# Optimization experiments

Measured on AMD Instinct MI355X. Metric: run time of the kernel, lower is better.

The kernel has to match this reference:

```python
import jax, jax.numpy as jnp
import numpy as np
from jax import lax

REPR, ACT, HID = 256, 2, 512
BN_EPS = 1e-5


def setup_inputs() -> dict:
    key = jax.random.key(0)
    ks = jax.random.split(key, 12)
    B, H, W, Tm1 = 512, 64, 64, 16
    d_in = REPR + ACT
    s = lambda k, shape, scale: jax.random.normal(k, shape, dtype=jnp.float32) * scale
    return {
        "init_state": jax.random.normal(ks[0], (B, 2, H, W), dtype=jnp.float32),
        "actions": jax.random.normal(ks[1], (B, Tm1, ACT), dtype=jnp.float32),
        "conv_w": s(ks[2], (16, 2, 3, 3), (1.0 / np.sqrt(2 * 9))),
        "bn_gamma": jnp.ones((16,), jnp.float32),
        "bn_beta": jnp.zeros((16,), jnp.float32),
        "enc_fc_w": s(ks[3], (REPR, 16), (1.0 / np.sqrt(16))),
        "enc_fc_b": s(ks[4], (REPR,), 0.01),
        "gru_w_ih": s(ks[5], (3 * HID, d_in), (1.0 / np.sqrt(HID))),
        "gru_w_hh": s(ks[6], (3 * HID, HID), (1.0 / np.sqrt(HID))),
        "gru_b_ih": s(ks[7], (3 * HID,), (1.0 / np.sqrt(HID))),
        "gru_b_hh": s(ks[8], (3 * HID,), (1.0 / np.sqrt(HID))),
        "pred_fc_w": s(ks[9], (REPR, HID), (1.0 / np.sqrt(HID))),
        "pred_fc_b": s(ks[10], (REPR,), 0.01),
    }


def _encoder(x, conv_w, bn_gamma, bn_beta, enc_fc_w, enc_fc_b):
    # Conv2d(2->16, 3x3, stride 1, pad 1, no bias), NCHW
    y = lax.conv_general_dilated(x, conv_w, (1, 1), "SAME",
                                 dimension_numbers=("NCHW", "OIHW", "NCHW"))
    # BatchNorm2d in training mode: batch statistics over (N, H, W)
    mean = jnp.mean(y, axis=(0, 2, 3), keepdims=True)
    var = jnp.var(y, axis=(0, 2, 3), keepdims=True)
    y = (y - mean) * lax.rsqrt(var + BN_EPS)
    y = y * bn_gamma[None, :, None, None] + bn_beta[None, :, None, None]
    y = jax.nn.relu(y)
    # MaxPool2d(2, 2)
    y = lax.reduce_window(y, -jnp.inf, lax.max, (1, 1, 2, 2), (1, 1, 2, 2), "VALID")
    # AdaptiveAvgPool2d((1,1)) + flatten
    y = jnp.mean(y, axis=(2, 3))  # (B, 16)
    return y @ enc_fc_w.T + enc_fc_b  # (B, repr_dim)


def reference(init_state, actions, conv_w, bn_gamma, bn_beta, enc_fc_w, enc_fc_b,
              gru_w_ih, gru_w_hh, gru_b_ih, gru_b_hh, pred_fc_w, pred_fc_b):
    B = init_state.shape[0]
    s0 = _encoder(init_state, conv_w, bn_gamma, bn_beta, enc_fc_w, enc_fc_b)  # (B, R)

    def step(carry, u_t):
        s_prev, h = carry
        x = jnp.concatenate([s_prev, u_t], axis=-1)          # (B, R+A)
        gx = x @ gru_w_ih.T + gru_b_ih                        # (B, 3H)
        gh = h @ gru_w_hh.T + gru_b_hh                        # (B, 3H)
        gx_r, gx_z, gx_n = jnp.split(gx, 3, axis=-1)
        gh_r, gh_z, gh_n = jnp.split(gh, 3, axis=-1)
        r = jax.nn.sigmoid(gx_r + gh_r)
        z = jax.nn.sigmoid(gx_z + gh_z)
        n = jnp.tanh(gx_n + r * gh_n)
        h_new = (1.0 - z) * n + z * h
        s_pred = jax.nn.relu(h_new @ pred_fc_w.T + pred_fc_b)  # (B, R)
        return (s_pred, h_new), s_pred

    h0 = jnp.zeros((B, HID), dtype=s0.dtype)
    u_seq = jnp.transpose(actions, (1, 0, 2))  # (T-1, B, A)
    _, preds = lax.scan(step, (s0, h0), u_seq)  # preds: (T-1, B, R)
    pred_encs = jnp.concatenate([s0[None], preds], axis=0)  # (T, B, R)
    return jnp.transpose(pred_encs, (1, 0, 2))  # (B, T, R)
```

## Files before the change

### kernel.cpp

```cpp
#include <hip/hip_runtime.h>
#include <hip/hip_bf16.h>
#include <math.h>

#define TM1 16
#define TT 17

typedef __attribute__((ext_vector_type(8))) __bf16 bf16x8;
typedef __attribute__((ext_vector_type(4))) float f32x4;

#define OFF_BSTATS 0
#define OFF_SPB    16384
#define OFF_PWB    81920
#define OFF_WIHB   147456
#define OFF_WHHB   344064
#define OFF_HB     737280

#define IMG_STRIDE 67
#define IMG_CI (66 * IMG_STRIDE)

__global__ __launch_bounds__(256) void enc_stats_prep(
    const float* __restrict__ x, const float* __restrict__ cw,
    float* __restrict__ bstats,
    const float* __restrict__ wih, const float* __restrict__ whh,
    const float* __restrict__ pw,
    __hip_bfloat16* __restrict__ wihb, __hip_bfloat16* __restrict__ whhb,
    __hip_bfloat16* __restrict__ pwb) {
  {
    const int n1 = 1536 * 256, n2 = 1536 * 512, n3 = 256 * 512;
    int i = blockIdx.x * 256 + threadIdx.x;
    int st = gridDim.x * 256;
    for (int j = i; j < n1 + n2 + n3; j += st) {
      if (j < n1) {
        int r = j >> 8, c = j & 255;
        wihb[j] = __float2bfloat16(wih[r * 258 + c]);
      } else if (j < n1 + n2) {
        int k = j - n1;
        whhb[k] = __float2bfloat16(whh[k]);
      } else {
        int k = j - n1 - n2;
        pwb[k] = __float2bfloat16(pw[k]);
      }
    }
  }

  __shared__ float imgp[2 * IMG_CI];
  __shared__ float reds[4][16], redq[4][16];
  const int b = blockIdx.x, tid = threadIdx.x;
  const int wv = tid >> 6;
  for (int i = tid; i < 2 * IMG_CI; i += 256) imgp[i] = 0.0f;
  __syncthreads();
  const float* xb = x + b * 8192;
  for (int i = tid; i < 8192; i += 256) {
    int ci = i >> 12, rem = i & 4095, y = rem >> 6, xx = rem & 63;
    imgp[ci * IMG_CI + (y + 1) * IMG_STRIDE + (xx + 1)] = xb[i];
  }
  __syncthreads();

  const int py = tid >> 3;
  const int cb = (tid & 7) << 3;

  float s[16], q[16];
#pragma unroll
  for (int c = 0; c < 16; ++c) { s[c] = 0.0f; q[c] = 0.0f; }

#pragma unroll 1
  for (int op = 0; op < 2; ++op) {
    const int ic = cb + 4 * op;
    float rv[2][4][6];
#pragma unroll
    for (int ci = 0; ci < 2; ++ci)
#pragma unroll
      for (int dy = 0; dy < 4; ++dy)
#pragma unroll
        for (int j = 0; j < 6; ++j)
          rv[ci][dy][j] = imgp[ci * IMG_CI + (2 * py + dy) * IMG_STRIDE + ic + j];
#pragma unroll
    for (int c4 = 0; c4 < 4; ++c4) {
      float a[4][8];
#pragma unroll
      for (int ch = 0; ch < 4; ++ch)
#pragma unroll
        for (int j = 0; j < 8; ++j) a[ch][j] = 0.0f;
#pragma unroll
      for (int ci = 0; ci < 2; ++ci) {
        float wk[4][9];
#pragma unroll
        for (int ch = 0; ch < 4; ++ch)
#pragma unroll
          for (int k = 0; k < 9; ++k)
            wk[ch][k] = cw[(c4 * 4 + ch) * 18 + ci * 9 + k];
#pragma unroll
        for (int ry = 0; ry < 2; ++ry)
#pragma unroll
          for (int rx = 0; rx < 4; ++rx)
#pragma unroll
            for (int ch = 0; ch < 4; ++ch) {
              float acc = a[ch][ry * 4 + rx];
#pragma unroll
              for (int dy = 0; dy < 3; ++dy) {
                acc = fmaf(wk[ch][dy * 3 + 0], rv[ci][ry + dy][rx + 0], acc);
                acc = fmaf(wk[ch][dy * 3 + 1], rv[ci][ry + dy][rx + 1], acc);
                acc = fmaf(wk[ch][dy * 3 + 2], rv[ci][ry + dy][rx + 2], acc);
              }
              a[ch][ry * 4 + rx] = acc;
            }
      }
#pragma unroll
      for (int ch = 0; ch < 4; ++ch)
#pragma unroll
        for (int j = 0; j < 8; ++j) {
          const float v = a[ch][j];
          s[c4 * 4 + ch] += v;
          q[c4 * 4 + ch] = fmaf(v, v, q[c4 * 4 + ch]);
        }
    }
  }

#pragma unroll
  for (int c = 0; c < 16; ++c) {
    float sv = s[c], qv = q[c];
#pragma unroll
    for (int off = 32; off >= 1; off >>= 1) {
      sv += __shfl_down(sv, off);
      qv += __shfl_down(qv, off);
    }
    if ((tid & 63) == 0) { reds[wv][c] = sv; redq[wv][c] = qv; }
  }
  __syncthreads();
  if (tid < 16)
    bstats[b * 32 + tid] = reds[0][tid] + reds[1][tid] + reds[2][tid] + reds[3][tid];
  else if (tid < 32) {
    int c = tid - 16;
    bstats[b * 32 + tid] = redq[0][c] + redq[1][c] + redq[2][c] + redq[3][c];
  }
}

__global__ __launch_bounds__(256) void enc_finish(const float* __restrict__ x,
                                                  const float* __restrict__ cw,
                                                  const float* __restrict__ bstats,
                                                  const float* __restrict__ gamma,
                                                  const float* __restrict__ beta,
                                                  const float* __restrict__ fcw,
                                                  const float* __restrict__ fcb,
                                                  __hip_bfloat16* __restrict__ spb,
                                                  float* __restrict__ out) {
  __shared__ float imgp[2 * IMG_CI];
  __shared__ float red[4][16];
  __shared__ float plds[16];
  __shared__ float statsL[32];
  __shared__ float racc[8][32];
  const int b = blockIdx.x, tid = threadIdx.x;
  const int wv = tid >> 6;

  {
    const int c = tid & 31, part = tid >> 5;
    float s = 0;
    for (int bb = part; bb < 512; bb += 8) s += bstats[bb * 32 + c];
    racc[part][c] = s;
  }
  for (int i = tid; i < 2 * IMG_CI; i += 256) imgp[i] = 0.0f;
  __syncthreads();
  if (tid < 32) {
    float v = 0;
#pragma unroll
    for (int p = 0; p < 8; ++p) v += racc[p][tid];
    statsL[tid] = v;
  }
  const float* xb = x + b * 8192;
  for (int i = tid; i < 8192; i += 256) {
    int ci = i >> 12, rem = i & 4095, y = rem >> 6, xx = rem & 63;
    imgp[ci * IMG_CI + (y + 1) * IMG_STRIDE + (xx + 1)] = xb[i];
  }
  __syncthreads();

  const float invN = 1.0f / (512.0f * 4096.0f);
  const int py = tid >> 3;
  const int cb = (tid & 7) << 3;

  float psum[16];
#pragma unroll
  for (int c = 0; c < 16; ++c) psum[c] = 0.0f;

#pragma unroll 1
  for (int op = 0; op < 2; ++op) {
    const int ic = cb + 4 * op;
    float rv[2][4][6];
#pragma unroll
    for (int ci = 0; ci < 2; ++ci)
#pragma unroll
      for (int dy = 0; dy < 4; ++dy)
#pragma unroll
        for (int j = 0; j < 6; ++j)
          rv[ci][dy][j] = imgp[ci * IMG_CI + (2 * py + dy) * IMG_STRIDE + ic + j];
#pragma unroll
    for (int c4 = 0; c4 < 4; ++c4) {
      float a[4][8];
#pragma unroll
      for (int ch = 0; ch < 4; ++ch)
#pragma unroll
        for (int j = 0; j < 8; ++j) a[ch][j] = 0.0f;
#pragma unroll
      for (int ci = 0; ci < 2; ++ci) {
        float wk[4][9];
#pragma unroll
        for (int ch = 0; ch < 4; ++ch)
#pragma unroll
          for (int k = 0; k < 9; ++k)
            wk[ch][k] = cw[(c4 * 4 + ch) * 18 + ci * 9 + k];
#pragma unroll
        for (int ry = 0; ry < 2; ++ry)
#pragma unroll
          for (int rx = 0; rx < 4; ++rx)
#pragma unroll
            for (int ch = 0; ch < 4; ++ch) {
              float acc = a[ch][ry * 4 + rx];
#pragma unroll
              for (int dy = 0; dy < 3; ++dy) {
                acc = fmaf(wk[ch][dy * 3 + 0], rv[ci][ry + dy][rx + 0], acc);
                acc = fmaf(wk[ch][dy * 3 + 1], rv[ci][ry + dy][rx + 1], acc);
                acc = fmaf(wk[ch][dy * 3 + 2], rv[ci][ry + dy][rx + 2], acc);
              }
              a[ch][ry * 4 + rx] = acc;
            }
      }
#pragma unroll
      for (int ch = 0; ch < 4; ++ch) {
        const int c = c4 * 4 + ch;
        const float m = statsL[c] * invN;
        const float var = statsL[16 + c] * invN - m * m;
        const float isd = rsqrtf(var + 1e-5f);
        const float sc = gamma[c] * isd;
        const float sh = beta[c] - m * sc;
#pragma unroll
        for (int j = 0; j < 2; ++j) {
          const float v00 = fmaxf(fmaf(a[ch][2 * j + 0], sc, sh), 0.0f);
          const float v01 = fmaxf(fmaf(a[ch][2 * j + 1], sc, sh), 0.0f);
          const float v10 = fmaxf(fmaf(a[ch][4 + 2 * j + 0], sc, sh), 0.0f);
          const float v11 = fmaxf(fmaf(a[ch][4 + 2 * j + 1], sc, sh), 0.0f);
          psum[c] += fmaxf(fmaxf(v00, v01), fmaxf(v10, v11));
        }
      }
    }
  }

#pragma unroll
  for (int c = 0; c < 16; ++c) {
    float v = psum[c];
#pragma unroll
    for (int off = 32; off >= 1; off >>= 1) v += __shfl_down(v, off);
    if ((tid & 63) == 0) red[wv][c] = v;
  }
  __syncthreads();
  if (tid < 16)
    plds[tid] = (red[0][tid] + red[1][tid] + red[2][tid] + red[3][tid]) * (1.0f / 1024.0f);
  __syncthreads();

  float acc = fcb[tid];
#pragma unroll
  for (int c = 0; c < 16; ++c) acc = fmaf(plds[c], fcw[tid * 16 + c], acc);
  spb[b * 256 + tid] = __float2bfloat16(acc);
  out[(b * TT + 0) * 256 + tid] = acc;
}

__global__ __launch_bounds__(384) void gru_v2(
    const __hip_bfloat16* __restrict__ spb,
    const __hip_bfloat16* __restrict__ hb_in,
    __hip_bfloat16* __restrict__ hb_out,
    const __hip_bfloat16* __restrict__ wihb,
    const __hip_bfloat16* __restrict__ whhb,
    const float* __restrict__ wih,
    const float* __restrict__ actions,
    const float* __restrict__ bih, const float* __restrict__ bhh,
    int t) {
  __shared__ __hip_bfloat16 sF[8 * 64 * 8];
  __shared__ __hip_bfloat16 hF[16 * 64 * 8];
  __shared__ float accL[4][2][256];
  const int tid = threadIdx.x;
  const int w = tid / 64, lane = tid & 63;
  const int l15 = lane & 15, hi = lane >> 4;
  const int cg = blockIdx.x, band = blockIdx.y;
  const int row0 = band * 16;
  const int ct = w & 1, g = w >> 1;

  for (int i = tid; i < 512; i += 384) {
    int kk = i >> 6, ln = i & 63;
    *(bf16x8*)(sF + i * 8) =
        *(const bf16x8*)(spb + (row0 + (ln & 15)) * 256 + kk * 32 + (ln >> 4) * 8);
  }
  if (t > 0) {
    for (int i = tid; i < 1024; i += 384) {
      int kk = i >> 6, ln = i & 63;
      *(bf16x8*)(hF + i * 8) =
          *(const bf16x8*)(hb_in + (row0 + (ln & 15)) * 512 + kk * 32 + (ln >> 4) * 8);
    }
  }
  __syncthreads();

  const int cj = cg * 32 + ct * 16;
  f32x4 accS = {0.f, 0.f, 0.f, 0.f}, accH = accS;
  {
    const __hip_bfloat16* B = wihb + (g * 512 + cj + l15) * 256 + hi * 8;
#pragma unroll
    for (int kk = 0; kk < 8; ++kk) {
      bf16x8 a = *(const bf16x8*)(sF + (kk * 64 + lane) * 8);
      accS = __builtin_amdgcn_mfma_f32_16x16x32_bf16(a, *(const bf16x8*)(B + kk * 32),
                                                     accS, 0, 0, 0);
    }
  }
  if (t > 0) {
    const __hip_bfloat16* B = whhb + (g * 512 + cj + l15) * 512 + hi * 8;
#pragma unroll
    for (int kk = 0; kk < 16; ++kk) {
      bf16x8 a = *(const bf16x8*)(hF + (kk * 64 + lane) * 8);
      accH = __builtin_amdgcn_mfma_f32_16x16x32_bf16(a, *(const bf16x8*)(B + kk * 32),
                                                     accH, 0, 0, 0);
    }
  }
  if (g < 2) {
#pragma unroll
    for (int i = 0; i < 4; ++i)
      accL[g][ct][(hi * 4 + i) * 16 + l15] = accS[i] + accH[i];
  } else {
#pragma unroll
    for (int i = 0; i < 4; ++i) {
      accL[2][ct][(hi * 4 + i) * 16 + l15] = accS[i];
      accL[3][ct][(hi * 4 + i) * 16 + l15] = accH[i];
    }
  }
  __syncthreads();

  if (w < 2) {
    f32x4 vR = *(const f32x4*)&accL[0][w][lane * 4];
    f32x4 vZ = *(const f32x4*)&accL[1][w][lane * 4];
    f32x4 vXN = *(const f32x4*)&accL[2][w][lane * 4];
    f32x4 vHN = *(const f32x4*)&accL[3][w][lane * 4];
    const int r = lane >> 2;
    const int row = row0 + r;
    const float u0 = actions[row * 32 + t * 2 + 0];
    const float u1 = actions[row * 32 + t * 2 + 1];
#pragma unroll
    for (int j = 0; j < 4; ++j) {
      const int c = (lane & 3) * 4 + j;
      const int col = cg * 32 + w * 16 + c;
      const float br = bih[col] + bhh[col];
      const float bz = bih[512 + col] + bhh[512 + col];
      const float bxn = bih[1024 + col];
      const float bhn = bhh[1024 + col];
      const float wur = wih[col * 258 + 256], wvr = wih[col * 258 + 257];
      const float wuz = wih[(512 + col) * 258 + 256], wvz = wih[(512 + col) * 258 + 257];
      const float wun = wih[(1024 + col) * 258 + 256], wvn = wih[(1024 + col) * 258 + 257];
      const float gr = vR[j] + br + u0 * wur + u1 * wvr;
      const float gz = vZ[j] + bz + u0 * wuz + u1 * wvz;
      const float gxn = vXN[j] + bxn + u0 * wun + u1 * wvn;
      const float ghn = vHN[j] + bhn;
      const float rg = 1.0f / (1.0f + __expf(-gr));
      const float zg = 1.0f / (1.0f + __expf(-gz));
      float xn = gxn + rg * ghn;
      xn = fminf(fmaxf(xn, -15.0f), 15.0f);
      const float e = __expf(2.0f * xn);
      const float ng = (e - 1.0f) / (e + 1.0f);
      const float hp = (t > 0) ? (float)hb_in[row * 512 + col] : 0.0f;
      const float hnv = (1.0f - zg) * ng + zg * hp;
      hb_out[row * 512 + col] = __float2bfloat16(hnv);
    }
  }
}

__global__ __launch_bounds__(256) void pred_v2(
    const __hip_bfloat16* __restrict__ hb,
    const __hip_bfloat16* __restrict__ pwb,
    const float* __restrict__ pb,
    float* __restrict__ out,
    __hip_bfloat16* __restrict__ spb,
    int slot) {
  __shared__ float accL[4][256];
  const int tid = threadIdx.x;
  const int w = tid >> 6, lane = tid & 63;
  const int l15 = lane & 15, hi = lane >> 4;
  const int pcg = blockIdx.x, band = blockIdx.y;
  const int row0 = band * 16, pc0 = pcg * 16;
  f32x4 acc = {0.f, 0.f, 0.f, 0.f};
  const __hip_bfloat16* A = hb + (row0 + l15) * 512 + w * 128 + hi * 8;
  const __hip_bfloat16* B = pwb + (pc0 + l15) * 512 + w * 128 + hi * 8;
#pragma unroll
  for (int kk = 0; kk < 4; ++kk)
    acc = __builtin_amdgcn_mfma_f32_16x16x32_bf16(*(const bf16x8*)(A + kk * 32),
                                                  *(const bf16x8*)(B + kk * 32),
                                                  acc, 0, 0, 0);
#pragma unroll
  for (int i = 0; i < 4; ++i) accL[w][(hi * 4 + i) * 16 + l15] = acc[i];
  __syncthreads();
  if (w == 0) {
    f32x4 p0 = *(const f32x4*)&accL[0][lane * 4];
    f32x4 p1 = *(const f32x4*)&accL[1][lane * 4];
    f32x4 p2 = *(const f32x4*)&accL[2][lane * 4];
    f32x4 p3 = *(const f32x4*)&accL[3][lane * 4];
    const int r = lane >> 2;
    const int row = row0 + r;
    float4 ov;
    float* po = &ov.x;
#pragma unroll
    for (int j = 0; j < 4; ++j) {
      const int c = (lane & 3) * 4 + j;
      const int col = pc0 + c;
      float v = p0[j] + p1[j] + p2[j] + p3[j] + pb[col];
      v = fmaxf(v, 0.0f);
      po[j] = v;
      spb[row * 256 + col] = __float2bfloat16(v);
    }
    *(float4*)(out + ((size_t)row * TT + slot) * 256 + pc0 + (lane & 3) * 4) = ov;
  }
}

extern "C" void kernel_launch(void* const* d_in, const int* in_sizes, int n_in,
                              void* d_out, int out_size, void* d_ws, size_t ws_size,
                              hipStream_t stream) {
  const float* x       = (const float*)d_in[0];
  const float* actions = (const float*)d_in[1];
  const float* cw      = (const float*)d_in[2];
  const float* gamma   = (const float*)d_in[3];
  const float* beta    = (const float*)d_in[4];
  const float* fcw     = (const float*)d_in[5];
  const float* fcb     = (const float*)d_in[6];
  const float* wih     = (const float*)d_in[7];
  const float* whh     = (const float*)d_in[8];
  const float* bih     = (const float*)d_in[9];
  const float* bhh     = (const float*)d_in[10];
  const float* pw      = (const float*)d_in[11];
  const float* pb      = (const float*)d_in[12];
  float* out = (float*)d_out;
  float* ws  = (float*)d_ws;

  float* bstats = ws + OFF_BSTATS;
  __hip_bfloat16* spb  = (__hip_bfloat16*)(ws + OFF_SPB);
  __hip_bfloat16* pwb  = (__hip_bfloat16*)(ws + OFF_PWB);
  __hip_bfloat16* wihb = (__hip_bfloat16*)(ws + OFF_WIHB);
  __hip_bfloat16* whhb = (__hip_bfloat16*)(ws + OFF_WHHB);
  __hip_bfloat16* hb0  = (__hip_bfloat16*)(ws + OFF_HB);
  __hip_bfloat16* hb1  = hb0 + 512 * 512;

  enc_stats_prep<<<dim3(512), dim3(256), 0, stream>>>(x, cw, bstats, wih, whh, pw,
                                                      wihb, whhb, pwb);
  enc_finish<<<dim3(512), dim3(256), 0, stream>>>(x, cw, bstats, gamma, beta, fcw, fcb,
                                                  spb, out);
  for (int t = 0; t < TM1; ++t) {
    __hip_bfloat16* hbi = (t & 1) ? hb1 : hb0;
    __hip_bfloat16* hbo = (t & 1) ? hb0 : hb1;
    gru_v2<<<dim3(16, 32), dim3(384), 0, stream>>>(spb, hbi, hbo, wihb, whhb,
                                                   wih, actions, bih, bhh, t);
    pred_v2<<<dim3(16, 32), dim3(256), 0, stream>>>(hbo, pwb, pb, out, spb, t + 1);
  }
}
```

Measured before the change: 364.1 us.

## Split encoder into row slabs, separate stats reduction, fuse encoder FC into first GRU step

```diff
diff --git a/kernel.cpp b/kernel.cpp
--- a/kernel.cpp
+++ b/kernel.cpp
@@ -9,14 +9,30 @@
 typedef __attribute__((ext_vector_type(4))) float f32x4;
 
 #define OFF_BSTATS 0
-#define OFF_SPB    16384
-#define OFF_PWB    81920
-#define OFF_WIHB   147456
-#define OFF_WHHB   344064
-#define OFF_HB     737280
+#define OFF_STATS  65536
+#define OFF_POOLED 65568
+#define OFF_SPB    98336
+#define OFF_PWB    163872
+#define OFF_WIHB   229408
+#define OFF_WHHB   426016
+#define OFF_HB     819232
 
 #define IMG_STRIDE 67
-#define IMG_CI (66 * IMG_STRIDE)
+#define SLAB_ROWS 18
+#define IMG_CI (SLAB_ROWS * IMG_STRIDE)
+
+__device__ __forceinline__ void stage_slab(float* __restrict__ imgp,
+                                           const float* __restrict__ xb, int slab, int tid) {
+  for (int i = tid; i < 2 * SLAB_ROWS * 66; i += 256) {
+    const int ci = i / (SLAB_ROWS * 66);
+    const int rem = i - ci * (SLAB_ROWS * 66);
+    const int lr = rem / 66, c = rem - lr * 66;
+    const int gr = slab * 16 - 1 + lr;
+    float v = 0.0f;
+    if (gr >= 0 && gr < 64 && c >= 1 && c <= 64) v = xb[ci * 4096 + gr * 64 + (c - 1)];
+    imgp[ci * IMG_CI + lr * IMG_STRIDE + c] = v;
+  }
+}
 
 __global__ __launch_bounds__(256) void enc_stats_prep(
     const float* __restrict__ x, const float* __restrict__ cw,
@@ -45,75 +61,67 @@
 
   __shared__ float imgp[2 * IMG_CI];
   __shared__ float reds[4][16], redq[4][16];
-  const int b = blockIdx.x, tid = threadIdx.x;
+  const int tid = threadIdx.x;
+  const int b = blockIdx.x >> 2, slab = blockIdx.x & 3;
   const int wv = tid >> 6;
-  for (int i = tid; i < 2 * IMG_CI; i += 256) imgp[i] = 0.0f;
-  __syncthreads();
-  const float* xb = x + b * 8192;
-  for (int i = tid; i < 8192; i += 256) {
-    int ci = i >> 12, rem = i & 4095, y = rem >> 6, xx = rem & 63;
-    imgp[ci * IMG_CI + (y + 1) * IMG_STRIDE + (xx + 1)] = xb[i];
-  }
-  __syncthreads();
-
-  const int py = tid >> 3;
-  const int cb = (tid & 7) << 3;
+  stage_slab(imgp, x + b * 8192, slab, tid);
+  __syncthreads();
+
+  const int pr = tid >> 5;
+  const int pc = tid & 31;
+
+  float rv[2][4][4];
+#pragma unroll
+  for (int ci = 0; ci < 2; ++ci)
+#pragma unroll
+    for (int dy = 0; dy < 4; ++dy)
+#pragma unroll
+      for (int j = 0; j < 4; ++j)
+        rv[ci][dy][j] = imgp[ci * IMG_CI + (2 * pr + dy) * IMG_STRIDE + 2 * pc + j];
 
   float s[16], q[16];
 #pragma unroll
   for (int c = 0; c < 16; ++c) { s[c] = 0.0f; q[c] = 0.0f; }
 
-#pragma unroll 1
-  for (int op = 0; op < 2; ++op) {
-    const int ic = cb + 4 * op;
-    float rv[2][4][6];
-#pragma unroll
-    for (int ci = 0; ci < 2; ++ci)
-#pragma unroll
-      for (int dy = 0; dy < 4; ++dy)
-#pragma unroll
-        for (int j = 0; j < 6; ++j)
-          rv[ci][dy][j] = imgp[ci * IMG_CI + (2 * py + dy) * IMG_STRIDE + ic + j];
-#pragma unroll
-    for (int c4 = 0; c4 < 4; ++c4) {
-      float a[4][8];
+#pragma unroll
+  for (int c4 = 0; c4 < 4; ++c4) {
+    float a[4][4];
+#pragma unroll
+    for (int ch = 0; ch < 4; ++ch)
+#pragma unroll
+      for (int p = 0; p < 4; ++p) a[ch][p] = 0.0f;
+#pragma unroll
+    for (int ci = 0; ci < 2; ++ci) {
+      float wk[4][9];
 #pragma unroll
       for (int ch = 0; ch < 4; ++ch)
 #pragma unroll
-        for (int j = 0; j < 8; ++j) a[ch][j] = 0.0f;
-#pragma unroll
-      for (int ci = 0; ci < 2; ++ci) {
-        float wk[4][9];
-#pragma unroll
-        for (int ch = 0; ch < 4; ++ch)
-#pragma unroll
-          for (int k = 0; k < 9; ++k)
-            wk[ch][k] = cw[(c4 * 4 + ch) * 18 + ci * 9 + k];
-#pragma unroll
-        for (int ry = 0; ry < 2; ++ry)
-#pragma unroll
-          for (int rx = 0; rx < 4; ++rx)
-#pragma unroll
-            for (int ch = 0; ch < 4; ++ch) {
-              float acc = a[ch][ry * 4 + rx];
-#pragma unroll
-              for (int dy = 0; dy < 3; ++dy) {
-                acc = fmaf(wk[ch][dy * 3 + 0], rv[ci][ry + dy][rx + 0], acc);
-                acc = fmaf(wk[ch][dy * 3 + 1], rv[ci][ry + dy][rx + 1], acc);
-                acc = fmaf(wk[ch][dy * 3 + 2], rv[ci][ry + dy][rx + 2], acc);
-              }
-              a[ch][ry * 4 + rx] = acc;
+        for (int k = 0; k < 9; ++k)
+          wk[ch][k] = cw[(c4 * 4 + ch) * 18 + ci * 9 + k];
+#pragma unroll
+      for (int ry = 0; ry < 2; ++ry)
+#pragma unroll
+        for (int rx = 0; rx < 2; ++rx)
+#pragma unroll
+          for (int ch = 0; ch < 4; ++ch) {
+            float acc = a[ch][ry * 2 + rx];
+#pragma unroll
+            for (int dy = 0; dy < 3; ++dy) {
+              acc = fmaf(wk[ch][dy * 3 + 0], rv[ci][ry + dy][rx + 0], acc);
+              acc = fmaf(wk[ch][dy * 3 + 1], rv[ci][ry + dy][rx + 1], acc);
+              acc = fmaf(wk[ch][dy * 3 + 2], rv[ci][ry + dy][rx + 2], acc);
             }
+            a[ch][ry * 2 + rx] = acc;
+          }
+    }
+#pragma unroll
+    for (int ch = 0; ch < 4; ++ch)
+#pragma unroll
+      for (int p = 0; p < 4; ++p) {
+        const float v = a[ch][p];
+        s[c4 * 4 + ch] += v;
+        q[c4 * 4 + ch] = fmaf(v, v, q[c4 * 4 + ch]);
       }
-#pragma unroll
-      for (int ch = 0; ch < 4; ++ch)
-#pragma unroll
-        for (int j = 0; j < 8; ++j) {
-          const float v = a[ch][j];
-          s[c4 * 4 + ch] += v;
-          q[c4 * 4 + ch] = fmaf(v, v, q[c4 * 4 + ch]);
-        }
-    }
   }
 
 #pragma unroll
@@ -128,118 +136,106 @@
   }
   __syncthreads();
   if (tid < 16)
-    bstats[b * 32 + tid] = reds[0][tid] + reds[1][tid] + reds[2][tid] + reds[3][tid];
+    bstats[blockIdx.x * 32 + tid] = reds[0][tid] + reds[1][tid] + reds[2][tid] + reds[3][tid];
   else if (tid < 32) {
     int c = tid - 16;
-    bstats[b * 32 + tid] = redq[0][c] + redq[1][c] + redq[2][c] + redq[3][c];
-  }
-}
-
-__global__ __launch_bounds__(256) void enc_finish(const float* __restrict__ x,
-                                                  const float* __restrict__ cw,
-                                                  const float* __restrict__ bstats,
-                                                  const float* __restrict__ gamma,
-                                                  const float* __restrict__ beta,
-                                                  const float* __restrict__ fcw,
-                                                  const float* __restrict__ fcb,
-                                                  __hip_bfloat16* __restrict__ spb,
-                                                  float* __restrict__ out) {
+    bstats[blockIdx.x * 32 + tid] = redq[0][c] + redq[1][c] + redq[2][c] + redq[3][c];
+  }
+}
+
+__global__ __launch_bounds__(256) void reduce_stats_k(const float* __restrict__ bstats,
+                                                      float* __restrict__ stats) {
+  __shared__ float acc[8][32];
+  const int c = threadIdx.x & 31, part = threadIdx.x >> 5;
+  float s = 0;
+  for (int i = part; i < 2048; i += 8) s += bstats[i * 32 + c];
+  acc[part][c] = s;
+  __syncthreads();
+  if (threadIdx.x < 32) {
+    float t = 0;
+#pragma unroll
+    for (int p = 0; p < 8; ++p) t += acc[p][threadIdx.x];
+    stats[threadIdx.x] = t;
+  }
+}
+
+__global__ __launch_bounds__(256) void enc_pool(const float* __restrict__ x,
+                                                const float* __restrict__ cw,
+                                                const float* __restrict__ stats,
+                                                const float* __restrict__ gamma,
+                                                const float* __restrict__ beta,
+                                                float* __restrict__ pooledG) {
   __shared__ float imgp[2 * IMG_CI];
   __shared__ float red[4][16];
-  __shared__ float plds[16];
   __shared__ float statsL[32];
-  __shared__ float racc[8][32];
-  const int b = blockIdx.x, tid = threadIdx.x;
+  const int tid = threadIdx.x;
+  const int b = blockIdx.x >> 2, slab = blockIdx.x & 3;
   const int wv = tid >> 6;
-
-  {
-    const int c = tid & 31, part = tid >> 5;
-    float s = 0;
-    for (int bb = part; bb < 512; bb += 8) s += bstats[bb * 32 + c];
-    racc[part][c] = s;
-  }
-  for (int i = tid; i < 2 * IMG_CI; i += 256) imgp[i] = 0.0f;
-  __syncthreads();
-  if (tid < 32) {
-    float v = 0;
-#pragma unroll
-    for (int p = 0; p < 8; ++p) v += racc[p][tid];
-    statsL[tid] = v;
-  }
-  const float* xb = x + b * 8192;
-  for (int i = tid; i < 8192; i += 256) {
-    int ci = i >> 12, rem = i & 4095, y = rem >> 6, xx = rem & 63;
-    imgp[ci * IMG_CI + (y + 1) * IMG_STRIDE + (xx + 1)] = xb[i];
-  }
+  stage_slab(imgp, x + b * 8192, slab, tid);
+  if (tid < 32) statsL[tid] = stats[tid];
   __syncthreads();
 
   const float invN = 1.0f / (512.0f * 4096.0f);
-  const int py = tid >> 3;
-  const int cb = (tid & 7) << 3;
+  const int pr = tid >> 5;
+  const int pc = tid & 31;
+
+  float rv[2][4][4];
+#pragma unroll
+  for (int ci = 0; ci < 2; ++ci)
+#pragma unroll
+    for (int dy = 0; dy < 4; ++dy)
+#pragma unroll
+      for (int j = 0; j < 4; ++j)
+        rv[ci][dy][j] = imgp[ci * IMG_CI + (2 * pr + dy) * IMG_STRIDE + 2 * pc + j];
 
   float psum[16];
 #pragma unroll
   for (int c = 0; c < 16; ++c) psum[c] = 0.0f;
 
-#pragma unroll 1
-  for (int op = 0; op < 2; ++op) {
-    const int ic = cb + 4 * op;
-    float rv[2][4][6];
-#pragma unroll
-    for (int ci = 0; ci < 2; ++ci)
-#pragma unroll
-      for (int dy = 0; dy < 4; ++dy)
-#pragma unroll
-        for (int j = 0; j < 6; ++j)
-          rv[ci][dy][j] = imgp[ci * IMG_CI + (2 * py + dy) * IMG_STRIDE + ic + j];
-#pragma unroll
-    for (int c4 = 0; c4 < 4; ++c4) {
-      float a[4][8];
+#pragma unroll
+  for (int c4 = 0; c4 < 4; ++c4) {
+    float a[4][4];
+#pragma unroll
+    for (int ch = 0; ch < 4; ++ch)
+#pragma unroll
+      for (int p = 0; p < 4; ++p) a[ch][p] = 0.0f;
+#pragma unroll
+    for (int ci = 0; ci < 2; ++ci) {
+      float wk[4][9];
 #pragma unroll
       for (int ch = 0; ch < 4; ++ch)
 #pragma unroll
-        for (int j = 0; j < 8; ++j) a[ch][j] = 0.0f;
-#pragma unroll
-      for (int ci = 0; ci < 2; ++ci) {
-        float wk[4][9];
-#pragma unroll
-        for (int ch = 0; ch < 4; ++ch)
-#pragma unroll
-          for (int k = 0; k < 9; ++k)
-            wk[ch][k] = cw[(c4 * 4 + ch) * 18 + ci * 9 + k];
-#pragma unroll
-        for (int ry = 0; ry < 2; ++ry)
-#pragma unroll
-          for (int rx = 0; rx < 4; ++rx)
-#pragma unroll
-            for (int ch = 0; ch < 4; ++ch) {
-              float acc = a[ch][ry * 4 + rx];
-#pragma unroll
-              for (int dy = 0; dy < 3; ++dy) {
-                acc = fmaf(wk[ch][dy * 3 + 0], rv[ci][ry + dy][rx + 0], acc);
-                acc = fmaf(wk[ch][dy * 3 + 1], rv[ci][ry + dy][rx + 1], acc);
-                acc = fmaf(wk[ch][dy * 3 + 2], rv[ci][ry + dy][rx + 2], acc);
-              }
-              a[ch][ry * 4 + rx] = acc;
+        for (int k = 0; k < 9; ++k)
+          wk[ch][k] = cw[(c4 * 4 + ch) * 18 + ci * 9 + k];
+#pragma unroll
+      for (int ry = 0; ry < 2; ++ry)
+#pragma unroll
+        for (int rx = 0; rx < 2; ++rx)
+#pragma unroll
+          for (int ch = 0; ch < 4; ++ch) {
+            float acc = a[ch][ry * 2 + rx];
+#pragma unroll
+            for (int dy = 0; dy < 3; ++dy) {
+              acc = fmaf(wk[ch][dy * 3 + 0], rv[ci][ry + dy][rx + 0], acc);
+              acc = fmaf(wk[ch][dy * 3 + 1], rv[ci][ry + dy][rx + 1], acc);
+              acc = fmaf(wk[ch][dy * 3 + 2], rv[ci][ry + dy][rx + 2], acc);
             }
-      }
-#pragma unroll
-      for (int ch = 0; ch < 4; ++ch) {
-        const int c = c4 * 4 + ch;
-        const float m = statsL[c] * invN;
-        const float var = statsL[16 + c] * invN - m * m;
-        const float isd = rsqrtf(var + 1e-5f);
-        const float sc = gamma[c] * isd;
-        const float sh = beta[c] - m * sc;
-#pragma unroll
-        for (int j = 0; j < 2; ++j) {
-          const float v00 = fmaxf(fmaf(a[ch][2 * j + 0], sc, sh), 0.0f);
-          const float v01 = fmaxf(fmaf(a[ch][2 * j + 1], sc, sh), 0.0f);
-          const float v10 = fmaxf(fmaf(a[ch][4 + 2 * j + 0], sc, sh), 0.0f);
-          const float v11 = fmaxf(fmaf(a[ch][4 + 2 * j + 1], sc, sh), 0.0f);
-          psum[c] += fmaxf(fmaxf(v00, v01), fmaxf(v10, v11));
-        }
-      }
+            a[ch][ry * 2 + rx] = acc;
+          }
+    }
+#pragma unroll
+    for (int ch = 0; ch < 4; ++ch) {
+      const int c = c4 * 4 + ch;
+      const float m = statsL[c] * invN;
+      const float var = statsL[16 + c] * invN - m * m;
+      const float isd = rsqrtf(var + 1e-5f);
+      const float sc = gamma[c] * isd;
+      const float sh = beta[c] - m * sc;
+      const float v0 = fmaxf(fmaf(a[ch][0], sc, sh), 0.0f);
+      const float v1 = fmaxf(fmaf(a[ch][1], sc, sh), 0.0f);
+      const float v2 = fmaxf(fmaf(a[ch][2], sc, sh), 0.0f);
+      const float v3 = fmaxf(fmaf(a[ch][3], sc, sh), 0.0f);
+      psum[c] += fmaxf(fmaxf(v0, v1), fmaxf(v2, v3));
     }
   }
 
@@ -252,14 +248,7 @@
   }
   __syncthreads();
   if (tid < 16)
-    plds[tid] = (red[0][tid] + red[1][tid] + red[2][tid] + red[3][tid]) * (1.0f / 1024.0f);
-  __syncthreads();
-
-  float acc = fcb[tid];
-#pragma unroll
-  for (int c = 0; c < 16; ++c) acc = fmaf(plds[c], fcw[tid * 16 + c], acc);
-  spb[b * 256 + tid] = __float2bfloat16(acc);
-  out[(b * TT + 0) * 256 + tid] = acc;
+    pooledG[blockIdx.x * 16 + tid] = red[0][tid] + red[1][tid] + red[2][tid] + red[3][tid];
 }
 
 __global__ __launch_bounds__(384) void gru_v2(
@@ -271,6 +260,10 @@
     const float* __restrict__ wih,
     const float* __restrict__ actions,
     const float* __restrict__ bih, const float* __restrict__ bhh,
+    const float* __restrict__ pooledG,
+    const float* __restrict__ fcw,
+    const float* __restrict__ fcb,
+    float* __restrict__ out,
     int t) {
   __shared__ __hip_bfloat16 sF[8 * 64 * 8];
   __shared__ __hip_bfloat16 hF[16 * 64 * 8];
@@ -282,12 +275,32 @@
   const int row0 = band * 16;
   const int ct = w & 1, g = w >> 1;
 
-  for (int i = tid; i < 512; i += 384) {
-    int kk = i >> 6, ln = i & 63;
-    *(bf16x8*)(sF + i * 8) =
-        *(const bf16x8*)(spb + (row0 + (ln & 15)) * 256 + kk * 32 + (ln >> 4) * 8);
-  }
-  if (t > 0) {
+  if (t == 0) {
+    float* avgF = &accL[0][0][0];
+    if (tid < 256) {
+      const int r = tid >> 4, k = tid & 15;
+      const int img = row0 + r;
+      const float v = pooledG[(img * 4 + 0) * 16 + k] + pooledG[(img * 4 + 1) * 16 + k] +
+                      pooledG[(img * 4 + 2) * 16 + k] + pooledG[(img * 4 + 3) * 16 + k];
+      avgF[r * 16 + k] = v * (1.0f / 1024.0f);
+    }
+    __syncthreads();
+    for (int i = tid; i < 4096; i += 384) {
+      const int kk = i >> 9, rem = i & 511, ln = rem >> 3, e = rem & 7;
+      const int r = ln & 15;
+      const int col = kk * 32 + (ln >> 4) * 8 + e;
+      float v = fcb[col];
+#pragma unroll
+      for (int k = 0; k < 16; ++k) v = fmaf(avgF[r * 16 + k], fcw[col * 16 + k], v);
+      sF[i] = __float2bfloat16(v);
+      if (cg == 0) out[((size_t)(row0 + r) * TT + 0) * 256 + col] = v;
+    }
+  } else {
+    for (int i = tid; i < 512; i += 384) {
+      int kk = i >> 6, ln = i & 63;
+      *(bf16x8*)(sF + i * 8) =
+          *(const bf16x8*)(spb + (row0 + (ln & 15)) * 256 + kk * 32 + (ln >> 4) * 8);
+    }
     for (int i = tid; i < 1024; i += 384) {
       int kk = i >> 6, ln = i & 63;
       *(bf16x8*)(hF + i * 8) =
@@ -316,6 +329,7 @@
                                                      accH, 0, 0, 0);
     }
   }
+  __syncthreads();
   if (g < 2) {
 #pragma unroll
     for (int i = 0; i < 4; ++i)
@@ -431,7 +445,9 @@
   float* out = (float*)d_out;
   float* ws  = (float*)d_ws;
 
-  float* bstats = ws + OFF_BSTATS;
+  float* bstats  = ws + OFF_BSTATS;
+  float* stats   = ws + OFF_STATS;
+  float* pooledG = ws + OFF_POOLED;
   __hip_bfloat16* spb  = (__hip_bfloat16*)(ws + OFF_SPB);
   __hip_bfloat16* pwb  = (__hip_bfloat16*)(ws + OFF_PWB);
   __hip_bfloat16* wihb = (__hip_bfloat16*)(ws + OFF_WIHB);
@@ -439,15 +455,16 @@
   __hip_bfloat16* hb0  = (__hip_bfloat16*)(ws + OFF_HB);
   __hip_bfloat16* hb1  = hb0 + 512 * 512;
 
-  enc_stats_prep<<<dim3(512), dim3(256), 0, stream>>>(x, cw, bstats, wih, whh, pw,
-                                                      wihb, whhb, pwb);
-  enc_finish<<<dim3(512), dim3(256), 0, stream>>>(x, cw, bstats, gamma, beta, fcw, fcb,
-                                                  spb, out);
+  enc_stats_prep<<<dim3(2048), dim3(256), 0, stream>>>(x, cw, bstats, wih, whh, pw,
+                                                       wihb, whhb, pwb);
+  reduce_stats_k<<<dim3(1), dim3(256), 0, stream>>>(bstats, stats);
+  enc_pool<<<dim3(2048), dim3(256), 0, stream>>>(x, cw, stats, gamma, beta, pooledG);
   for (int t = 0; t < TM1; ++t) {
     __hip_bfloat16* hbi = (t & 1) ? hb1 : hb0;
     __hip_bfloat16* hbo = (t & 1) ? hb0 : hb1;
     gru_v2<<<dim3(16, 32), dim3(384), 0, stream>>>(spb, hbi, hbo, wihb, whhb,
-                                                   wih, actions, bih, bhh, t);
+                                                   wih, actions, bih, bhh,
+                                                   pooledG, fcw, fcb, out, t);
     pred_v2<<<dim3(16, 32), dim3(256), 0, stream>>>(hbo, pwb, pb, out, spb, t + 1);
   }
 }
```

Result: slower. 414.3 us (+13.8%).
